# Performance work log

Measured on AMD Instinct MI355X. Metric: run time of the kernel, lower is better.

The kernel has to match this reference:

```python
import jax, jax.numpy as jnp
import numpy as np

N = 500_000
E = 8_000_000
DIM = 3
CG_ITERS = 20
CG_TOL = 1e-4


def setup_inputs() -> dict:
    key = jax.random.key(0)
    k0, k1, k2, k3, k4, k5 = jax.random.split(key, 6)
    u_hat = jax.random.normal(k0, (N, DIM), dtype=jnp.float32)
    edge_index = jax.random.randint(k1, (2, E), 0, N, dtype=jnp.int32)
    face_normals = jax.random.normal(k2, (E, DIM), dtype=jnp.float32)
    face_areas = jax.random.uniform(k3, (E,), dtype=jnp.float32)
    face_dists = jax.random.uniform(k4, (E,), dtype=jnp.float32)
    cell_volumes = jax.random.uniform(k5, (N,), dtype=jnp.float32)
    return {
        "u_hat": u_hat,
        "edge_index": edge_index,
        "face_normals": face_normals,
        "face_areas": face_areas,
        "face_dists": face_dists,
        "cell_volumes": cell_volumes,
    }


def _segsum(vals, idx, n):
    return jax.ops.segment_sum(vals, idx, num_segments=n)


def reference(u_hat, edge_index, face_normals, face_areas, face_dists, cell_volumes):
    src, dst = edge_index[0], edge_index[1]
    n = u_hat.shape[0]

    # --- compute_divergence: D_i = (1/V_i) sum flux over faces into i ---
    u_face = 0.5 * (u_hat[src] + u_hat[dst])                 # (E, dim)
    flux = jnp.sum(u_face * face_normals, axis=-1) * face_areas  # (E,)
    div = _segsum(flux, dst, n) / jnp.clip(cell_volumes, 1e-12)

    # --- build_laplacian_rhs ---
    w = face_areas / jnp.clip(face_dists, 1e-8)              # (E,)
    diag = _segsum(w, dst, n)                                # (N,)
    off = -w
    b = div

    # --- cg_solve with Jacobi preconditioner ---
    m_inv = 1.0 / jnp.clip(diag, 1e-8)

    def matvec(phi):
        return diag * phi + _segsum(off * phi[src], dst, n)

    phi0 = jnp.zeros_like(b)
    r0 = b - matvec(phi0)
    z0 = m_inv * r0
    p0 = z0
    rz0 = jnp.sum(r0 * z0)

    def step(state, _):
        phi, r, z, p, rz, done = state
        # torch checks ||r|| < tol and breaks before the update
        active = jnp.logical_and(~done, jnp.linalg.norm(r) >= CG_TOL)
        ap = matvec(p)
        alpha = rz / (jnp.sum(p * ap) + 1e-12)
        phi_n = phi + alpha * p
        r_n = r - alpha * ap
        z_n = m_inv * r_n
        rz_n = jnp.sum(r_n * z_n)
        beta = rz_n / (rz + 1e-12)
        p_n = z_n + beta * p
        sel = lambda a, b_: jnp.where(active, a, b_)
        new_state = (sel(phi_n, phi), sel(r_n, r), sel(z_n, z),
                     sel(p_n, p), jnp.where(active, rz_n, rz), ~active)
        return new_state, None

    (phi, _, _, _, _, _), _ = jax.lax.scan(
        step, (phi0, r0, z0, p0, rz0, jnp.array(False)), None, length=CG_ITERS)

    # --- apply_pressure_correction ---
    grad_term = (w * phi[src])[:, None] * face_normals       # (E, dim)
    grad_phi = _segsum(grad_term, dst, n) / jnp.clip(cell_volumes, 1e-12)[:, None]
    u_corrected = u_hat - grad_phi
    return u_corrected, phi
```

## Files before the change

### kernel.cpp

```cpp
#include <hip/hip_runtime.h>


#define TPB 256
#define TPB_A 1024
#define KB 2048
#define NBLK 256
#define MAXNB 2048
#define CG_ITERS 20
#define TOL2 1e-8f

struct Sum3 { float a, b, c; };

__device__ inline Sum3 block_sum3_bcast(const float* __restrict__ A,
                                        const float* __restrict__ B,
                                        const float* __restrict__ C, int n) {
  float va = 0.f, vb = 0.f, vc = 0.f;
  for (int k = threadIdx.x; k < n; k += TPB) { va += A[k]; vb += B[k]; vc += C[k]; }
#pragma unroll
  for (int o = 32; o; o >>= 1) {
    va += __shfl_down(va, o, 64);
    vb += __shfl_down(vb, o, 64);
    vc += __shfl_down(vc, o, 64);
  }
  __shared__ float sa[TPB / 64], sb[TPB / 64], sc[TPB / 64], bc[3];
  int lane = threadIdx.x & 63, wid = threadIdx.x >> 6;
  if (lane == 0) { sa[wid] = va; sb[wid] = vb; sc[wid] = vc; }
  __syncthreads();
  if (threadIdx.x == 0) {
    float ta = 0.f, tb = 0.f, tc = 0.f;
#pragma unroll
    for (int k = 0; k < TPB / 64; k++) { ta += sa[k]; tb += sb[k]; tc += sc[k]; }
    bc[0] = ta; bc[1] = tb; bc[2] = tc;
  }
  __syncthreads();
  Sum3 r{bc[0], bc[1], bc[2]};
  __syncthreads();
  return r;
}

__device__ inline void block_reduce1_store(float v1, float* d1) {
#pragma unroll
  for (int o = 32; o; o >>= 1) v1 += __shfl_down(v1, o, 64);
  __shared__ float s1[TPB / 64];
  int lane = threadIdx.x & 63, wid = threadIdx.x >> 6;
  if (lane == 0) s1[wid] = v1;
  __syncthreads();
  if (threadIdx.x == 0) {
    float t1 = 0.f;
#pragma unroll
    for (int k = 0; k < TPB / 64; k++) t1 += s1[k];
    *d1 = t1;
  }
}

__device__ inline void block_reduce2_store(float v1, float v2, float* d1, float* d2) {
#pragma unroll
  for (int o = 32; o; o >>= 1) {
    v1 += __shfl_down(v1, o, 64);
    v2 += __shfl_down(v2, o, 64);
  }
  __shared__ float s1[TPB / 64], s2[TPB / 64];
  int lane = threadIdx.x & 63, wid = threadIdx.x >> 6;
  if (lane == 0) { s1[wid] = v1; s2[wid] = v2; }
  __syncthreads();
  if (threadIdx.x == 0) {
    float t1 = 0.f, t2 = 0.f;
#pragma unroll
    for (int k = 0; k < TPB / 64; k++) { t1 += s1[k]; t2 += s2[k]; }
    *d1 = t1;
    *d2 = t2;
  }
}

__global__ __launch_bounds__(TPB_A) void bucket_hist(
    const int* __restrict__ ei, unsigned* __restrict__ mat,
    int E, int NB, int chunk) {
  __shared__ unsigned cntL[MAXNB];
  for (int i = threadIdx.x; i < NB; i += TPB_A) cntL[i] = 0;
  __syncthreads();
  int blk = blockIdx.x;
  int e0 = blk * chunk, e1 = min(E, e0 + chunk);
  for (int e = e0 + threadIdx.x; e < e1; e += TPB_A)
    atomicAdd(&cntL[((unsigned)ei[E + e]) >> 8], 1u);
  __syncthreads();
  for (int b = threadIdx.x; b < NB; b += TPB_A)
    mat[(size_t)b * NBLK + blk] = cntL[b];
}

__global__ __launch_bounds__(TPB) void scan_blocks(
    const unsigned* __restrict__ cnt, unsigned* __restrict__ offs,
    unsigned* __restrict__ btot, int n) {
  __shared__ unsigned sd[TPB];
  int t = threadIdx.x;
  int base = blockIdx.x * 1024 + t * 4;
  unsigned v0 = 0, v1 = 0, v2 = 0, v3 = 0;
  if (base + 0 < n) v0 = cnt[base + 0];
  if (base + 1 < n) v1 = cnt[base + 1];
  if (base + 2 < n) v2 = cnt[base + 2];
  if (base + 3 < n) v3 = cnt[base + 3];
  unsigned local = v0 + v1 + v2 + v3;
  sd[t] = local;
  __syncthreads();
  for (int o = 1; o < TPB; o <<= 1) {
    unsigned x = (t >= o) ? sd[t - o] : 0u;
    __syncthreads();
    sd[t] += x;
    __syncthreads();
  }
  unsigned excl = sd[t] - local;
  if (base + 0 < n) offs[base + 0] = excl; excl += v0;
  if (base + 1 < n) offs[base + 1] = excl; excl += v1;
  if (base + 2 < n) offs[base + 2] = excl; excl += v2;
  if (base + 3 < n) offs[base + 3] = excl;
  if (t == TPB - 1) btot[blockIdx.x] = sd[TPB - 1];
}

__global__ __launch_bounds__(512) void scan_totals(unsigned* __restrict__ btot, int nb) {
  __shared__ unsigned sd[512];
  int t = threadIdx.x;
  unsigned v = (t < nb) ? btot[t] : 0u;
  sd[t] = v;
  __syncthreads();
  for (int o = 1; o < 512; o <<= 1) {
    unsigned x = (t >= o) ? sd[t - o] : 0u;
    __syncthreads();
    sd[t] += x;
    __syncthreads();
  }
  if (t < nb) btot[t] = sd[t] - v;
}

__global__ __launch_bounds__(TPB) void scan_add(
    unsigned* __restrict__ offs, const unsigned* __restrict__ btot,
    int n, unsigned total) {
  int i = blockIdx.x * TPB + threadIdx.x;
  if (i < n) offs[i] += btot[i >> 10];
  if (i == 0) offs[n] = total;
}

__global__ __launch_bounds__(TPB_A) void bucket_place(
    const int* __restrict__ ei, const float* __restrict__ u_hat,
    const float* __restrict__ fn, const float* __restrict__ fa,
    const float* __restrict__ fd, const unsigned* __restrict__ offs,
    unsigned long long* __restrict__ A1, float* __restrict__ A2flux,
    int* __restrict__ A3eid, int E, int NB, int chunk) {
  __shared__ unsigned cntL[MAXNB];
  __shared__ unsigned offL[MAXNB];
  int blk = blockIdx.x;
  for (int i = threadIdx.x; i < NB; i += TPB_A) {
    cntL[i] = 0;
    offL[i] = offs[(size_t)i * NBLK + blk];
  }
  __syncthreads();
  int e0 = blk * chunk, e1 = min(E, e0 + chunk);
  for (int e = e0 + threadIdx.x; e < e1; e += TPB_A) {
    int s = ei[e], d = ei[E + e];
    float area = fa[e];
    float w = area / fmaxf(fd[e], 1e-8f);
    float ux = 0.5f * (u_hat[3 * s]     + u_hat[3 * d]);
    float uy = 0.5f * (u_hat[3 * s + 1] + u_hat[3 * d + 1]);
    float uz = 0.5f * (u_hat[3 * s + 2] + u_hat[3 * d + 2]);
    float flux = (ux * fn[3 * e] + uy * fn[3 * e + 1] + uz * fn[3 * e + 2]) * area;
    unsigned b = ((unsigned)d) >> 8;
    unsigned dl = ((unsigned)d) & 255u;
    unsigned r = atomicAdd(&cntL[b], 1u);
    unsigned pos = offL[b] + r;
    unsigned hi = (dl << 19) | (unsigned)s;
    A1[pos] = ((unsigned long long)hi << 32) | (unsigned long long)__float_as_uint(w);
    A2flux[pos] = flux;
    A3eid[pos] = e;
  }
}

__global__ __launch_bounds__(TPB) void node_setup(
    const unsigned long long* __restrict__ A1, const float* __restrict__ A2flux,
    const unsigned* __restrict__ offs, const float* __restrict__ cv,
    float* __restrict__ diag, float* __restrict__ r, float* __restrict__ p,
    float* __restrict__ phi, float* __restrict__ minv,
    float* __restrict__ rz_part, float* __restrict__ rr_part, int N, int NB) {
  __shared__ float wacc[256], facc[256];
  int b = blockIdx.x;
  float rzv = 0.f, rrv = 0.f;
  if (b < NB) {
    wacc[threadIdx.x] = 0.f;
    facc[threadIdx.x] = 0.f;
    __syncthreads();
    unsigned jb = offs[(size_t)b * NBLK], je = offs[(size_t)(b + 1) * NBLK];
    for (unsigned j = jb + threadIdx.x; j < je; j += TPB) {
      unsigned long long v = A1[j];
      unsigned hi = (unsigned)(v >> 32);
      float w = __uint_as_float((unsigned)v);
      atomicAdd(&wacc[hi >> 19], w);
      atomicAdd(&facc[hi >> 19], A2flux[j]);
    }
    __syncthreads();
    int node = (b << 8) + threadIdx.x;
    if (node < N) {
      float wsum = wacc[threadIdx.x];
      float vol = fmaxf(cv[node], 1e-12f);
      float bval = facc[threadIdx.x] / vol;
      float mi = 1.0f / fmaxf(wsum, 1e-8f);
      diag[node] = wsum;
      minv[node] = mi;
      r[node] = bval;
      phi[node] = 0.f;
      float pi = mi * bval;
      p[node] = pi;
      rzv = bval * pi;
      rrv = bval * bval;
    }
  }
  block_reduce2_store(rzv, rrv, &rz_part[blockIdx.x], &rr_part[blockIdx.x]);
}

__global__ __launch_bounds__(TPB) void matvec(
    const float* __restrict__ p, const float* __restrict__ diag,
    const unsigned* __restrict__ offs, const unsigned long long* __restrict__ A1,
    float* __restrict__ ap, float* __restrict__ pap_part, int N, int NB) {
  __shared__ float acc[256];
  int b = blockIdx.x;
  float contrib = 0.f;
  if (b < NB) {
    acc[threadIdx.x] = 0.f;
    __syncthreads();
    unsigned jb = offs[(size_t)b * NBLK], je = offs[(size_t)(b + 1) * NBLK];
    for (unsigned j = jb + threadIdx.x; j < je; j += TPB) {
      unsigned long long v = A1[j];
      unsigned hi = (unsigned)(v >> 32);
      float w = __uint_as_float((unsigned)v);
      atomicAdd(&acc[hi >> 19], w * p[hi & 0x7FFFFu]);
    }
    __syncthreads();
    int node = (b << 8) + threadIdx.x;
    if (node < N) {
      float pi = p[node];
      float api = diag[node] * pi - acc[threadIdx.x];
      ap[node] = api;
      contrib = pi * api;
    }
  }
  block_reduce1_store(contrib, &pap_part[blockIdx.x]);
}

__global__ __launch_bounds__(TPB) void cg_update(
    float* __restrict__ phi, float* __restrict__ r, const float* __restrict__ p,
    const float* __restrict__ ap, const float* __restrict__ minv,
    const float* __restrict__ pap_it, const float* __restrict__ rz_it,
    const float* __restrict__ rr_it, float* __restrict__ rz_next,
    float* __restrict__ rr_next, int N) {
  Sum3 s = block_sum3_bcast(pap_it, rz_it, rr_it, KB);
  bool act = (s.c >= TOL2);
  float alpha = s.b / (s.a + 1e-12f);
  float rzacc = 0.f, rracc = 0.f;
  for (int i = blockIdx.x * TPB + threadIdx.x; i < N; i += KB * TPB) {
    float ri = r[i];
    if (act) {
      phi[i] += alpha * p[i];
      ri -= alpha * ap[i];
      r[i] = ri;
    }
    float zi = minv[i] * ri;
    rzacc += ri * zi;
    rracc += ri * ri;
  }
  block_reduce2_store(rzacc, rracc, &rz_next[blockIdx.x], &rr_next[blockIdx.x]);
}

__global__ __launch_bounds__(TPB) void p_update(
    float* __restrict__ p, const float* __restrict__ r,
    const float* __restrict__ minv, const float* __restrict__ rz_next,
    const float* __restrict__ rz_it, const float* __restrict__ rr_it, int N) {
  Sum3 s = block_sum3_bcast(rz_next, rz_it, rr_it, KB);
  if (s.c < TOL2) return;
  float beta = s.a / (s.b + 1e-12f);
  for (int i = blockIdx.x * TPB + threadIdx.x; i < N; i += KB * TPB) {
    p[i] = minv[i] * r[i] + beta * p[i];
  }
}

__global__ __launch_bounds__(TPB) void finalize(
    const float* __restrict__ u_hat, const float* __restrict__ cv,
    const float* __restrict__ phi, const unsigned* __restrict__ offs,
    const unsigned long long* __restrict__ A1, const int* __restrict__ A3eid,
    const float* __restrict__ fn, float* __restrict__ out, int N, int NB) {
  __shared__ float gxa[256], gya[256], gza[256];
  int b = blockIdx.x;
  if (b >= NB) return;
  gxa[threadIdx.x] = 0.f;
  gya[threadIdx.x] = 0.f;
  gza[threadIdx.x] = 0.f;
  __syncthreads();
  unsigned jb = offs[(size_t)b * NBLK], je = offs[(size_t)(b + 1) * NBLK];
  for (unsigned j = jb + threadIdx.x; j < je; j += TPB) {
    unsigned long long v = A1[j];
    unsigned hi = (unsigned)(v >> 32);
    float w = __uint_as_float((unsigned)v);
    float t = w * phi[hi & 0x7FFFFu];
    int e = A3eid[j];
    int dl = hi >> 19;
    atomicAdd(&gxa[dl], t * fn[3 * e]);
    atomicAdd(&gya[dl], t * fn[3 * e + 1]);
    atomicAdd(&gza[dl], t * fn[3 * e + 2]);
  }
  __syncthreads();
  int node = (b << 8) + threadIdx.x;
  if (node < N) {
    float iv = 1.0f / fmaxf(cv[node], 1e-12f);
    out[3 * node]     = u_hat[3 * node]     - gxa[threadIdx.x] * iv;
    out[3 * node + 1] = u_hat[3 * node + 1] - gya[threadIdx.x] * iv;
    out[3 * node + 2] = u_hat[3 * node + 2] - gza[threadIdx.x] * iv;
    out[3 * N + node] = phi[node];
  }
}

extern "C" void kernel_launch(void* const* d_in, const int* in_sizes, int n_in,
                              void* d_out, int out_size, void* d_ws, size_t ws_size,
                              hipStream_t stream) {
  const float* u_hat = (const float*)d_in[0];
  const int*   ei    = (const int*)d_in[1];
  const float* fn    = (const float*)d_in[2];
  const float* fa    = (const float*)d_in[3];
  const float* fd    = (const float*)d_in[4];
  const float* cv    = (const float*)d_in[5];
  float* out = (float*)d_out;

  const int N = in_sizes[0] / 3;
  const int E = in_sizes[1] / 2;
  const int NB = (N + 255) >> 8;
  const int NS = NB * NBLK;
  const int chunk = (E + NBLK - 1) / NBLK;

  char* base = (char*)d_ws;
  size_t off = 0;
  auto alloc = [&](size_t bytes) -> void* {
    void* ptr = base + off;
    off = (off + bytes + 255) & ~size_t(255);
    return ptr;
  };
  unsigned* mat   = (unsigned*)alloc((size_t)NS * 4);
  unsigned* offs  = (unsigned*)alloc((size_t)(NS + 1) * 4);
  unsigned* btot  = (unsigned*)alloc(512 * 4);
  float*    diag  = (float*)alloc((size_t)N * 4);
  float*    minv  = (float*)alloc((size_t)N * 4);
  float*    phi   = (float*)alloc((size_t)N * 4);
  float*    rvec  = (float*)alloc((size_t)N * 4);
  float*    pvec  = (float*)alloc((size_t)N * 4);
  float*    ap    = (float*)alloc((size_t)N * 4);
  float*    rzrr  = (float*)alloc((size_t)(2 * (CG_ITERS + 1)) * KB * 4);
  float*    papp  = (float*)alloc((size_t)CG_ITERS * KB * 4);
  unsigned long long* A1 = (unsigned long long*)alloc((size_t)E * 8);
  float*    A2flux = (float*)alloc((size_t)E * 4);
  int*      A3eid  = (int*)alloc((size_t)E * 4);
  (void)ws_size; (void)n_in; (void)out_size;

  auto rz_part = [&](int it) { return rzrr + (size_t)(2 * it) * KB; };
  auto rr_part = [&](int it) { return rzrr + (size_t)(2 * it + 1) * KB; };
  auto pap_part = [&](int it) { return papp + (size_t)it * KB; };

  const int nbScan = (NS + 1023) / 1024;
  const int gridScanAdd = (NS + TPB - 1) / TPB;

  bucket_hist<<<NBLK, TPB_A, 0, stream>>>(ei, mat, E, NB, chunk);

  scan_blocks<<<nbScan, TPB, 0, stream>>>(mat, offs, btot, NS);
  scan_totals<<<1, 512, 0, stream>>>(btot, nbScan);
  scan_add<<<gridScanAdd, TPB, 0, stream>>>(offs, btot, NS, (unsigned)E);

  bucket_place<<<NBLK, TPB_A, 0, stream>>>(ei, u_hat, fn, fa, fd, offs,
                                           A1, A2flux, A3eid, E, NB, chunk);

  node_setup<<<KB, TPB, 0, stream>>>(A1, A2flux, offs, cv, diag,
                                     rvec, pvec, phi, minv,
                                     rz_part(0), rr_part(0), N, NB);

  for (int it = 0; it < CG_ITERS; it++) {
    matvec<<<KB, TPB, 0, stream>>>(pvec, diag, offs, A1, ap,
                                   pap_part(it), N, NB);
    cg_update<<<KB, TPB, 0, stream>>>(phi, rvec, pvec, ap, minv,
                                      pap_part(it), rz_part(it), rr_part(it),
                                      rz_part(it + 1), rr_part(it + 1), N);
    if (it < CG_ITERS - 1) {
      p_update<<<KB, TPB, 0, stream>>>(pvec, rvec, minv,
                                       rz_part(it + 1), rz_part(it),
                                       rr_part(it), N);
    }
  }

  finalize<<<NB, TPB, 0, stream>>>(u_hat, cv, phi, offs, A1, A3eid,
                                   fn, out, N, NB);
}
```

Baseline: 2.516 ms.

## Widen destination buckets to 512 nodes and pack flux with edge id

```diff
diff --git a/kernel.cpp b/kernel.cpp
--- a/kernel.cpp
+++ b/kernel.cpp
@@ -2,10 +2,11 @@
 
 
 #define TPB 256
+#define TPB_B 512
 #define TPB_A 1024
 #define KB 2048
 #define NBLK 256
-#define MAXNB 2048
+#define MAXNB 1024
 #define CG_ITERS 20
 #define TOL2 1e-8f
 
@@ -38,35 +39,37 @@
   return r;
 }
 
+template <int BS>
 __device__ inline void block_reduce1_store(float v1, float* d1) {
 #pragma unroll
   for (int o = 32; o; o >>= 1) v1 += __shfl_down(v1, o, 64);
-  __shared__ float s1[TPB / 64];
+  __shared__ float s1[BS / 64];
   int lane = threadIdx.x & 63, wid = threadIdx.x >> 6;
   if (lane == 0) s1[wid] = v1;
   __syncthreads();
   if (threadIdx.x == 0) {
     float t1 = 0.f;
 #pragma unroll
-    for (int k = 0; k < TPB / 64; k++) t1 += s1[k];
+    for (int k = 0; k < BS / 64; k++) t1 += s1[k];
     *d1 = t1;
   }
 }
 
+template <int BS>
 __device__ inline void block_reduce2_store(float v1, float v2, float* d1, float* d2) {
 #pragma unroll
   for (int o = 32; o; o >>= 1) {
     v1 += __shfl_down(v1, o, 64);
     v2 += __shfl_down(v2, o, 64);
   }
-  __shared__ float s1[TPB / 64], s2[TPB / 64];
+  __shared__ float s1[BS / 64], s2[BS / 64];
   int lane = threadIdx.x & 63, wid = threadIdx.x >> 6;
   if (lane == 0) { s1[wid] = v1; s2[wid] = v2; }
   __syncthreads();
   if (threadIdx.x == 0) {
     float t1 = 0.f, t2 = 0.f;
 #pragma unroll
-    for (int k = 0; k < TPB / 64; k++) { t1 += s1[k]; t2 += s2[k]; }
+    for (int k = 0; k < BS / 64; k++) { t1 += s1[k]; t2 += s2[k]; }
     *d1 = t1;
     *d2 = t2;
   }
@@ -81,7 +84,7 @@
   int blk = blockIdx.x;
   int e0 = blk * chunk, e1 = min(E, e0 + chunk);
   for (int e = e0 + threadIdx.x; e < e1; e += TPB_A)
-    atomicAdd(&cntL[((unsigned)ei[E + e]) >> 8], 1u);
+    atomicAdd(&cntL[((unsigned)ei[E + e]) >> 9], 1u);
   __syncthreads();
   for (int b = threadIdx.x; b < NB; b += TPB_A)
     mat[(size_t)b * NBLK + blk] = cntL[b];
@@ -142,8 +145,8 @@
     const int* __restrict__ ei, const float* __restrict__ u_hat,
     const float* __restrict__ fn, const float* __restrict__ fa,
     const float* __restrict__ fd, const unsigned* __restrict__ offs,
-    unsigned long long* __restrict__ A1, float* __restrict__ A2flux,
-    int* __restrict__ A3eid, int E, int NB, int chunk) {
+    unsigned long long* __restrict__ A1, int2* __restrict__ A2,
+    int E, int NB, int chunk) {
   __shared__ unsigned cntL[MAXNB];
   __shared__ unsigned offL[MAXNB];
   int blk = blockIdx.x;
@@ -161,24 +164,23 @@
     float uy = 0.5f * (u_hat[3 * s + 1] + u_hat[3 * d + 1]);
     float uz = 0.5f * (u_hat[3 * s + 2] + u_hat[3 * d + 2]);
     float flux = (ux * fn[3 * e] + uy * fn[3 * e + 1] + uz * fn[3 * e + 2]) * area;
-    unsigned b = ((unsigned)d) >> 8;
-    unsigned dl = ((unsigned)d) & 255u;
+    unsigned b = ((unsigned)d) >> 9;
+    unsigned dl = ((unsigned)d) & 511u;
     unsigned r = atomicAdd(&cntL[b], 1u);
     unsigned pos = offL[b] + r;
     unsigned hi = (dl << 19) | (unsigned)s;
     A1[pos] = ((unsigned long long)hi << 32) | (unsigned long long)__float_as_uint(w);
-    A2flux[pos] = flux;
-    A3eid[pos] = e;
-  }
-}
-
-__global__ __launch_bounds__(TPB) void node_setup(
-    const unsigned long long* __restrict__ A1, const float* __restrict__ A2flux,
+    A2[pos] = make_int2(e, __float_as_int(flux));
+  }
+}
+
+__global__ __launch_bounds__(TPB_B) void node_setup(
+    const unsigned long long* __restrict__ A1, const int2* __restrict__ A2,
     const unsigned* __restrict__ offs, const float* __restrict__ cv,
     float* __restrict__ diag, float* __restrict__ r, float* __restrict__ p,
     float* __restrict__ phi, float* __restrict__ minv,
     float* __restrict__ rz_part, float* __restrict__ rr_part, int N, int NB) {
-  __shared__ float wacc[256], facc[256];
+  __shared__ float wacc[TPB_B], facc[TPB_B];
   int b = blockIdx.x;
   float rzv = 0.f, rrv = 0.f;
   if (b < NB) {
@@ -186,15 +188,15 @@
     facc[threadIdx.x] = 0.f;
     __syncthreads();
     unsigned jb = offs[(size_t)b * NBLK], je = offs[(size_t)(b + 1) * NBLK];
-    for (unsigned j = jb + threadIdx.x; j < je; j += TPB) {
+    for (unsigned j = jb + threadIdx.x; j < je; j += TPB_B) {
       unsigned long long v = A1[j];
       unsigned hi = (unsigned)(v >> 32);
       float w = __uint_as_float((unsigned)v);
       atomicAdd(&wacc[hi >> 19], w);
-      atomicAdd(&facc[hi >> 19], A2flux[j]);
-    }
-    __syncthreads();
-    int node = (b << 8) + threadIdx.x;
+      atomicAdd(&facc[hi >> 19], __int_as_float(A2[j].y));
+    }
+    __syncthreads();
+    int node = (b << 9) + threadIdx.x;
     if (node < N) {
       float wsum = wacc[threadIdx.x];
       float vol = fmaxf(cv[node], 1e-12f);
@@ -210,28 +212,28 @@
       rrv = bval * bval;
     }
   }
-  block_reduce2_store(rzv, rrv, &rz_part[blockIdx.x], &rr_part[blockIdx.x]);
-}
-
-__global__ __launch_bounds__(TPB) void matvec(
+  block_reduce2_store<TPB_B>(rzv, rrv, &rz_part[blockIdx.x], &rr_part[blockIdx.x]);
+}
+
+__global__ __launch_bounds__(TPB_B) void matvec(
     const float* __restrict__ p, const float* __restrict__ diag,
     const unsigned* __restrict__ offs, const unsigned long long* __restrict__ A1,
     float* __restrict__ ap, float* __restrict__ pap_part, int N, int NB) {
-  __shared__ float acc[256];
+  __shared__ float acc[TPB_B];
   int b = blockIdx.x;
   float contrib = 0.f;
   if (b < NB) {
     acc[threadIdx.x] = 0.f;
     __syncthreads();
     unsigned jb = offs[(size_t)b * NBLK], je = offs[(size_t)(b + 1) * NBLK];
-    for (unsigned j = jb + threadIdx.x; j < je; j += TPB) {
+    for (unsigned j = jb + threadIdx.x; j < je; j += TPB_B) {
       unsigned long long v = A1[j];
       unsigned hi = (unsigned)(v >> 32);
       float w = __uint_as_float((unsigned)v);
       atomicAdd(&acc[hi >> 19], w * p[hi & 0x7FFFFu]);
     }
     __syncthreads();
-    int node = (b << 8) + threadIdx.x;
+    int node = (b << 9) + threadIdx.x;
     if (node < N) {
       float pi = p[node];
       float api = diag[node] * pi - acc[threadIdx.x];
@@ -239,7 +241,7 @@
       contrib = pi * api;
     }
   }
-  block_reduce1_store(contrib, &pap_part[blockIdx.x]);
+  block_reduce1_store<TPB_B>(contrib, &pap_part[blockIdx.x]);
 }
 
 __global__ __launch_bounds__(TPB) void cg_update(
@@ -263,7 +265,7 @@
     rzacc += ri * zi;
     rracc += ri * ri;
   }
-  block_reduce2_store(rzacc, rracc, &rz_next[blockIdx.x], &rr_next[blockIdx.x]);
+  block_reduce2_store<TPB>(rzacc, rracc, &rz_next[blockIdx.x], &rr_next[blockIdx.x]);
 }
 
 __global__ __launch_bounds__(TPB) void p_update(
@@ -278,12 +280,12 @@
   }
 }
 
-__global__ __launch_bounds__(TPB) void finalize(
+__global__ __launch_bounds__(TPB_B) void finalize(
     const float* __restrict__ u_hat, const float* __restrict__ cv,
     const float* __restrict__ phi, const unsigned* __restrict__ offs,
-    const unsigned long long* __restrict__ A1, const int* __restrict__ A3eid,
+    const unsigned long long* __restrict__ A1, const int2* __restrict__ A2,
     const float* __restrict__ fn, float* __restrict__ out, int N, int NB) {
-  __shared__ float gxa[256], gya[256], gza[256];
+  __shared__ float gxa[TPB_B], gya[TPB_B], gza[TPB_B];
   int b = blockIdx.x;
   if (b >= NB) return;
   gxa[threadIdx.x] = 0.f;
@@ -291,19 +293,19 @@
   gza[threadIdx.x] = 0.f;
   __syncthreads();
   unsigned jb = offs[(size_t)b * NBLK], je = offs[(size_t)(b + 1) * NBLK];
-  for (unsigned j = jb + threadIdx.x; j < je; j += TPB) {
+  for (unsigned j = jb + threadIdx.x; j < je; j += TPB_B) {
     unsigned long long v = A1[j];
     unsigned hi = (unsigned)(v >> 32);
     float w = __uint_as_float((unsigned)v);
     float t = w * phi[hi & 0x7FFFFu];
-    int e = A3eid[j];
+    int e = A2[j].x;
     int dl = hi >> 19;
     atomicAdd(&gxa[dl], t * fn[3 * e]);
     atomicAdd(&gya[dl], t * fn[3 * e + 1]);
     atomicAdd(&gza[dl], t * fn[3 * e + 2]);
   }
   __syncthreads();
-  int node = (b << 8) + threadIdx.x;
+  int node = (b << 9) + threadIdx.x;
   if (node < N) {
     float iv = 1.0f / fmaxf(cv[node], 1e-12f);
     out[3 * node]     = u_hat[3 * node]     - gxa[threadIdx.x] * iv;
@@ -326,7 +328,7 @@
 
   const int N = in_sizes[0] / 3;
   const int E = in_sizes[1] / 2;
-  const int NB = (N + 255) >> 8;
+  const int NB = (N + 511) >> 9;
   const int NS = NB * NBLK;
   const int chunk = (E + NBLK - 1) / NBLK;
 
@@ -349,8 +351,7 @@
   float*    rzrr  = (float*)alloc((size_t)(2 * (CG_ITERS + 1)) * KB * 4);
   float*    papp  = (float*)alloc((size_t)CG_ITERS * KB * 4);
   unsigned long long* A1 = (unsigned long long*)alloc((size_t)E * 8);
-  float*    A2flux = (float*)alloc((size_t)E * 4);
-  int*      A3eid  = (int*)alloc((size_t)E * 4);
+  int2*     A2    = (int2*)alloc((size_t)E * 8);
   (void)ws_size; (void)n_in; (void)out_size;
 
   auto rz_part = [&](int it) { return rzrr + (size_t)(2 * it) * KB; };
@@ -367,15 +368,15 @@
   scan_add<<<gridScanAdd, TPB, 0, stream>>>(offs, btot, NS, (unsigned)E);
 
   bucket_place<<<NBLK, TPB_A, 0, stream>>>(ei, u_hat, fn, fa, fd, offs,
-                                           A1, A2flux, A3eid, E, NB, chunk);
-
-  node_setup<<<KB, TPB, 0, stream>>>(A1, A2flux, offs, cv, diag,
-                                     rvec, pvec, phi, minv,
-                                     rz_part(0), rr_part(0), N, NB);
+                                           A1, A2, E, NB, chunk);
+
+  node_setup<<<KB, TPB_B, 0, stream>>>(A1, A2, offs, cv, diag,
+                                       rvec, pvec, phi, minv,
+                                       rz_part(0), rr_part(0), N, NB);
 
   for (int it = 0; it < CG_ITERS; it++) {
-    matvec<<<KB, TPB, 0, stream>>>(pvec, diag, offs, A1, ap,
-                                   pap_part(it), N, NB);
+    matvec<<<KB, TPB_B, 0, stream>>>(pvec, diag, offs, A1, ap,
+                                     pap_part(it), N, NB);
     cg_update<<<KB, TPB, 0, stream>>>(phi, rvec, pvec, ap, minv,
                                       pap_part(it), rz_part(it), rr_part(it),
                                       rz_part(it + 1), rr_part(it + 1), N);
@@ -386,6 +387,6 @@
     }
   }
 
-  finalize<<<NB, TPB, 0, stream>>>(u_hat, cv, phi, offs, A1, A3eid,
-                                   fn, out, N, NB);
-}
+  finalize<<<NB, TPB_B, 0, stream>>>(u_hat, cv, phi, offs, A1, A2,
+                                     fn, out, N, NB);
+}
```

New measurement: 2.304 ms. 1.09x faster.
